# Kernel optimization log

Hardware: AMD Instinct MI355X
Metric: run time of the kernel (lower is better)

Reference implementation:

```python
import jax, jax.numpy as jnp
import numpy as np

N_ATOM_TYPES = 100
N_BOND_TYPES = 10
N_NODES = 10000
N_EDGES = 320000
N_CAND = 100000
HID = 256
N_MP = 3


def setup_inputs() -> dict:
    key = jax.random.key(0)
    ks = jax.random.split(key, 16)
    d = HID
    inp = {
        "atom_types": jax.random.randint(ks[0], (N_NODES,), 0, N_ATOM_TYPES),
        "bond_types": jax.random.randint(ks[1], (N_EDGES,), 0, N_BOND_TYPES),
        "edge_index": jax.random.randint(ks[2], (2, N_EDGES), 0, N_NODES),
        "candidates": jax.random.randint(ks[3], (N_CAND, 2), 0, N_NODES),
        # parameters (weights stored as [in, out]; bias [out])
        "atom_embed": jax.random.normal(ks[4], (N_ATOM_TYPES, d)) * 0.02,
        "atom_W": jax.random.normal(ks[5], (d, d)) / np.sqrt(d),
        "atom_b": jnp.zeros((d,)),
        "bond_embed": jax.random.normal(ks[6], (N_BOND_TYPES, d)) * 0.02,
        "bond_W": jax.random.normal(ks[7], (d, d)) / np.sqrt(d),
        "bond_b": jnp.zeros((d,)),
        "conv_W": jax.random.normal(ks[8], (N_MP, d, d)) / np.sqrt(d),
        "conv_b": jnp.zeros((N_MP, d)),
        "s_W1": jax.random.normal(ks[9], (2 * d, d)) / np.sqrt(2 * d),
        "s_b1": jnp.zeros((d,)),
        "s_W2": jax.random.normal(ks[10], (d, 1)) / np.sqrt(d),
        "s_b2": jnp.zeros((1,)),
    }
    return inp


def _wln_forward(atom_types, bond_types, edge_index, candidates,
                 atom_embed, atom_W, atom_b, bond_embed, bond_W, bond_b,
                 conv_W, conv_b, s_W1, s_b1, s_W2, s_b2):
    # encoders
    h = atom_embed[atom_types] @ atom_W + atom_b            # [N, d]
    e = bond_embed[bond_types] @ bond_W + bond_b            # [E, d] (unused downstream, as in the original forward)
    del e

    src, dst = edge_index[0], edge_index[1]
    n = h.shape[0]
    ones = jnp.ones((src.shape[0],), dtype=h.dtype)
    deg_out = jax.ops.segment_sum(ones, src, num_segments=n)
    deg_in = jax.ops.segment_sum(ones, dst, num_segments=n)
    norm_src = jnp.where(deg_out > 0, deg_out ** -0.5, 0.0)[:, None]  # [N,1]
    norm_dst = jnp.where(deg_in > 0, deg_in ** -0.5, 0.0)[:, None]

    # message passing: DGL GraphConv norm='both' + ReLU
    for i in range(conv_W.shape[0]):
        m = (h * norm_src)[src]                             # [E, d]
        agg = jax.ops.segment_sum(m, dst, num_segments=n)   # [N, d]
        h = jax.nn.relu((agg * norm_dst) @ conv_W[i] + conv_b[i])

    # batched candidate scorer: gather + concat + 2-layer MLP
    u, v = candidates[:, 0], candidates[:, 1]
    pair = jnp.concatenate([h[u], h[v]], axis=-1)           # [C, 2d]
    hid = jax.nn.relu(pair @ s_W1 + s_b1)                   # [C, d]
    scores = hid @ s_W2 + s_b2                              # [C, 1]
    return scores.squeeze(-1)                               # [C]


def reference(atom_types, bond_types, edge_index, candidates,
              atom_embed, atom_W, atom_b, bond_embed, bond_W, bond_b,
              conv_W, conv_b, s_W1, s_b1, s_W2, s_b2):
    return _wln_forward(atom_types, bond_types, edge_index, candidates,
                        atom_embed, atom_W, atom_b, bond_embed, bond_W, bond_b,
                        conv_W, conv_b, s_W1, s_b1, s_W2, s_b2)
```

## Files before the change

kernel.cpp:

```cpp
#include <hip/hip_runtime.h>

#define N_NODES 10000
#define N_EDGES 320000
#define N_CAND  100000
#define HID     256
#define N_MP    3
#define N_ATYPE 100

typedef short bf16x8 __attribute__((ext_vector_type(8)));
typedef float f32x4  __attribute__((ext_vector_type(4)));

static __device__ __forceinline__ float relu_f(float x) { return x > 0.f ? x : 0.f; }

static __device__ __forceinline__ void split_bf16(float s, unsigned short& hi,
                                                  unsigned short& lo)
{
    unsigned u = __float_as_uint(s);
    hi = (unsigned short)(u >> 16);
    float rem = s - __uint_as_float(u & 0xffff0000u);
    unsigned v = __float_as_uint(rem);
    unsigned r = v + 0x7fffu + ((v >> 16) & 1u);
    lo = (unsigned short)(r >> 16);
}

static __device__ __forceinline__ void mfma_tile(
    const unsigned short* __restrict__ Ah, const unsigned short* __restrict__ Al,
    const unsigned short* __restrict__ Wh, const unsigned short* __restrict__ Wl,
    const float* __restrict__ bias, const float* __restrict__ scale,
    float* __restrict__ outF, unsigned short* __restrict__ outH,
    unsigned short* __restrict__ outL,
    int M, int mb, int nb, int doRelu)
{
    int l  = threadIdx.x & 63;
    int li = l & 15;
    int g  = l >> 4;

    int r0 = mb + li;       if (r0 >= M) r0 = M - 1;
    int r1 = mb + 16 + li;  if (r1 >= M) r1 = M - 1;
    int c0 = nb + li;
    int c1 = nb + 16 + li;

    const unsigned short* pA0h = Ah + (size_t)r0 * 256 + g * 8;
    const unsigned short* pA1h = Ah + (size_t)r1 * 256 + g * 8;
    const unsigned short* pA0l = Al + (size_t)r0 * 256 + g * 8;
    const unsigned short* pA1l = Al + (size_t)r1 * 256 + g * 8;
    const unsigned short* pB0h = Wh + (size_t)c0 * 256 + g * 8;
    const unsigned short* pB1h = Wh + (size_t)c1 * 256 + g * 8;
    const unsigned short* pB0l = Wl + (size_t)c0 * 256 + g * 8;
    const unsigned short* pB1l = Wl + (size_t)c1 * 256 + g * 8;

    f32x4 acc00 = {0.f, 0.f, 0.f, 0.f};
    f32x4 acc01 = {0.f, 0.f, 0.f, 0.f};
    f32x4 acc10 = {0.f, 0.f, 0.f, 0.f};
    f32x4 acc11 = {0.f, 0.f, 0.f, 0.f};

    #pragma unroll
    for (int ks = 0; ks < 8; ++ks) {
        int o = ks * 32;
        bf16x8 a0h = *(const bf16x8*)(pA0h + o);
        bf16x8 a1h = *(const bf16x8*)(pA1h + o);
        bf16x8 a0l = *(const bf16x8*)(pA0l + o);
        bf16x8 a1l = *(const bf16x8*)(pA1l + o);
        bf16x8 b0h = *(const bf16x8*)(pB0h + o);
        bf16x8 b1h = *(const bf16x8*)(pB1h + o);
        bf16x8 b0l = *(const bf16x8*)(pB0l + o);
        bf16x8 b1l = *(const bf16x8*)(pB1l + o);

        acc00 = __builtin_amdgcn_mfma_f32_16x16x32_bf16(a0h, b0h, acc00, 0, 0, 0);
        acc01 = __builtin_amdgcn_mfma_f32_16x16x32_bf16(a0h, b1h, acc01, 0, 0, 0);
        acc10 = __builtin_amdgcn_mfma_f32_16x16x32_bf16(a1h, b0h, acc10, 0, 0, 0);
        acc11 = __builtin_amdgcn_mfma_f32_16x16x32_bf16(a1h, b1h, acc11, 0, 0, 0);

        acc00 = __builtin_amdgcn_mfma_f32_16x16x32_bf16(a0h, b0l, acc00, 0, 0, 0);
        acc01 = __builtin_amdgcn_mfma_f32_16x16x32_bf16(a0h, b1l, acc01, 0, 0, 0);
        acc10 = __builtin_amdgcn_mfma_f32_16x16x32_bf16(a1h, b0l, acc10, 0, 0, 0);
        acc11 = __builtin_amdgcn_mfma_f32_16x16x32_bf16(a1h, b1l, acc11, 0, 0, 0);

        acc00 = __builtin_amdgcn_mfma_f32_16x16x32_bf16(a0l, b0h, acc00, 0, 0, 0);
        acc01 = __builtin_amdgcn_mfma_f32_16x16x32_bf16(a0l, b1h, acc01, 0, 0, 0);
        acc10 = __builtin_amdgcn_mfma_f32_16x16x32_bf16(a1l, b0h, acc10, 0, 0, 0);
        acc11 = __builtin_amdgcn_mfma_f32_16x16x32_bf16(a1l, b1h, acc11, 0, 0, 0);
    }

    #pragma unroll
    for (int rt = 0; rt < 2; ++rt) {
        #pragma unroll
        for (int ct = 0; ct < 2; ++ct) {
            f32x4 a = rt ? (ct ? acc11 : acc10) : (ct ? acc01 : acc00);
            int col = nb + ct * 16 + li;
            float bv = bias ? bias[col] : 0.f;
            #pragma unroll
            for (int j = 0; j < 4; ++j) {
                int row = mb + rt * 16 + g * 4 + j;
                if (row >= M) continue;
                float v = a[j] + bv;
                if (doRelu) v = relu_f(v);
                if (scale) v *= scale[row];
                if (outF) {
                    outF[(size_t)row * 256 + col] = v;
                } else {
                    unsigned short hi, lo;
                    split_bf16(v, hi, lo);
                    outH[(size_t)row * 256 + col] = hi;
                    outL[(size_t)row * 256 + col] = lo;
                }
            }
        }
    }
}

static __device__ __forceinline__ void mfma_tile_e0(
    const float* __restrict__ A, const float* __restrict__ B,
    const float* __restrict__ bias, float* __restrict__ C,
    int M, int mb, int nb)
{
    int l  = threadIdx.x & 63;
    int li = l & 15;
    int g  = l >> 4;

    int r0 = mb + li;       if (r0 >= M) r0 = M - 1;
    int r1 = mb + 16 + li;  if (r1 >= M) r1 = M - 1;
    int c0 = nb + li;
    int c1 = nb + 16 + li;

    f32x4 acc00 = {0.f, 0.f, 0.f, 0.f};
    f32x4 acc01 = {0.f, 0.f, 0.f, 0.f};
    f32x4 acc10 = {0.f, 0.f, 0.f, 0.f};
    f32x4 acc11 = {0.f, 0.f, 0.f, 0.f};

    #pragma unroll
    for (int ks = 0; ks < 8; ++ks) {
        int k0 = ks * 32 + g * 8;
        float av0[8], av1[8];
        {
            float4 x0 = *(const float4*)(A + (size_t)r0 * 256 + k0);
            float4 x1 = *(const float4*)(A + (size_t)r0 * 256 + k0 + 4);
            av0[0]=x0.x; av0[1]=x0.y; av0[2]=x0.z; av0[3]=x0.w;
            av0[4]=x1.x; av0[5]=x1.y; av0[6]=x1.z; av0[7]=x1.w;
            float4 y0 = *(const float4*)(A + (size_t)r1 * 256 + k0);
            float4 y1 = *(const float4*)(A + (size_t)r1 * 256 + k0 + 4);
            av1[0]=y0.x; av1[1]=y0.y; av1[2]=y0.z; av1[3]=y0.w;
            av1[4]=y1.x; av1[5]=y1.y; av1[6]=y1.z; av1[7]=y1.w;
        }
        float bv0[8], bv1[8];
        #pragma unroll
        for (int j = 0; j < 8; ++j) {
            bv0[j] = B[(size_t)(k0 + j) * 256 + c0];
            bv1[j] = B[(size_t)(k0 + j) * 256 + c1];
        }
        bf16x8 a0h, a0l, a1h, a1l, b0h, b0l, b1h, b1l;
        #pragma unroll
        for (int j = 0; j < 8; ++j) {
            unsigned short h, lo;
            split_bf16(av0[j], h, lo); a0h[j] = (short)h; a0l[j] = (short)lo;
            split_bf16(av1[j], h, lo); a1h[j] = (short)h; a1l[j] = (short)lo;
            split_bf16(bv0[j], h, lo); b0h[j] = (short)h; b0l[j] = (short)lo;
            split_bf16(bv1[j], h, lo); b1h[j] = (short)h; b1l[j] = (short)lo;
        }

        acc00 = __builtin_amdgcn_mfma_f32_16x16x32_bf16(a0h, b0h, acc00, 0, 0, 0);
        acc01 = __builtin_amdgcn_mfma_f32_16x16x32_bf16(a0h, b1h, acc01, 0, 0, 0);
        acc10 = __builtin_amdgcn_mfma_f32_16x16x32_bf16(a1h, b0h, acc10, 0, 0, 0);
        acc11 = __builtin_amdgcn_mfma_f32_16x16x32_bf16(a1h, b1h, acc11, 0, 0, 0);

        acc00 = __builtin_amdgcn_mfma_f32_16x16x32_bf16(a0h, b0l, acc00, 0, 0, 0);
        acc01 = __builtin_amdgcn_mfma_f32_16x16x32_bf16(a0h, b1l, acc01, 0, 0, 0);
        acc10 = __builtin_amdgcn_mfma_f32_16x16x32_bf16(a1h, b0l, acc10, 0, 0, 0);
        acc11 = __builtin_amdgcn_mfma_f32_16x16x32_bf16(a1h, b1l, acc11, 0, 0, 0);

        acc00 = __builtin_amdgcn_mfma_f32_16x16x32_bf16(a0l, b0h, acc00, 0, 0, 0);
        acc01 = __builtin_amdgcn_mfma_f32_16x16x32_bf16(a0l, b1h, acc01, 0, 0, 0);
        acc10 = __builtin_amdgcn_mfma_f32_16x16x32_bf16(a1l, b0h, acc10, 0, 0, 0);
        acc11 = __builtin_amdgcn_mfma_f32_16x16x32_bf16(a1l, b1h, acc11, 0, 0, 0);
    }

    #pragma unroll
    for (int rt = 0; rt < 2; ++rt) {
        #pragma unroll
        for (int ct = 0; ct < 2; ++ct) {
            f32x4 a = rt ? (ct ? acc11 : acc10) : (ct ? acc01 : acc00);
            int col = nb + ct * 16 + li;
            float bv = bias[col];
            #pragma unroll
            for (int j = 0; j < 4; ++j) {
                int row = mb + rt * 16 + g * 4 + j;
                if (row >= M) continue;
                C[(size_t)row * 256 + col] = a[j] + bv;
            }
        }
    }
}

__global__ __launch_bounds__(256) void k_prep(
    const float* __restrict__ conv_W, const float* __restrict__ s_W1,
    const float* __restrict__ atom_embed, const float* __restrict__ atom_W,
    const float* __restrict__ atom_b,
    unsigned short* __restrict__ WTh, unsigned short* __restrict__ WTl,
    float* __restrict__ E0)
{
    int bid = blockIdx.x;
    if (bid < 80) {
        __shared__ float T[64][65];
        int mat = bid >> 4;
        int t   = bid & 15;
        int ti  = t >> 2;
        int tj  = t & 3;
        const float* src = (mat < 3) ? conv_W + (size_t)mat * 65536
                                     : s_W1 + (size_t)(mat - 3) * 65536;
        #pragma unroll
        for (int i = 0; i < 16; ++i) {
            int flat = i * 256 + threadIdx.x;
            int kr = flat >> 6;
            int nc = flat & 63;
            T[kr][nc] = src[(size_t)(ti * 64 + kr) * 256 + tj * 64 + nc];
        }
        __syncthreads();
        #pragma unroll
        for (int i = 0; i < 16; ++i) {
            int flat = i * 256 + threadIdx.x;
            int nr = flat >> 6;
            int kc = flat & 63;
            unsigned short hi, lo;
            split_bf16(T[kc][nr], hi, lo);
            size_t oi = (size_t)mat * 65536 +
                        (size_t)(tj * 64 + nr) * 256 + ti * 64 + kc;
            WTh[oi] = hi;
            WTl[oi] = lo;
        }
        return;
    }
    int w = (bid - 80) * 4 + (threadIdx.x >> 6);
    if (w < 32) {
        int x = w >> 3, y = w & 7;
        mfma_tile_e0(atom_embed, atom_W, atom_b, E0, N_ATYPE, x * 32, y * 32);
    }
}

__global__ void k_hist(const int* __restrict__ ei,
                       int* __restrict__ dout, int* __restrict__ din)
{
    int e = blockIdx.x * blockDim.x + threadIdx.x;
    if (e >= N_EDGES) return;
    atomicAdd(&dout[ei[e]], 1);
    atomicAdd(&din[ei[N_EDGES + e]], 1);
}

__global__ __launch_bounds__(256) void k_nhs(
    const int* __restrict__ types, const float* __restrict__ E0,
    const int* __restrict__ dout, const int* __restrict__ din,
    float* __restrict__ ns, float* __restrict__ nd, float* __restrict__ h,
    int* __restrict__ off)
{
    if (blockIdx.x == 2500) {
        __shared__ int part[256];
        int t = threadIdx.x;
        const int chunk = 40;
        int base = t * chunk;
        int s = 0;
        for (int i = 0; i < chunk; ++i) {
            int idx = base + i;
            if (idx < N_NODES) s += din[idx];
        }
        part[t] = s;
        __syncthreads();
        for (int d = 1; d < 256; d <<= 1) {
            int v = (t >= d) ? part[t - d] : 0;
            __syncthreads();
            part[t] += v;
            __syncthreads();
        }
        int run = (t == 0) ? 0 : part[t - 1];
        if (t == 0) off[0] = 0;
        for (int i = 0; i < chunk; ++i) {
            int idx = base + i;
            if (idx < N_NODES) { run += din[idx]; off[idx + 1] = run; }
        }
        return;
    }
    int node = blockIdx.x * 4 + (threadIdx.x >> 6);
    int lane = threadIdx.x & 63;
    if (node >= N_NODES) return;
    int o  = dout[node];
    int in = din[node];
    float nsv = (o  > 0) ? (1.0f / sqrtf((float)o))  : 0.f;
    float ndv = (in > 0) ? (1.0f / sqrtf((float)in)) : 0.f;
    if (lane == 0) { ns[node] = nsv; nd[node] = ndv; }
    int t = types[node];
    float4 v = ((const float4*)E0)[(size_t)t * 64 + lane];
    v.x *= nsv; v.y *= nsv; v.z *= nsv; v.w *= nsv;
    ((float4*)h)[(size_t)node * 64 + lane] = v;
}

__global__ void k_fill(const int* __restrict__ ei, const int* __restrict__ off,
                       int* __restrict__ cur, int* __restrict__ csr)
{
    int e = blockIdx.x * blockDim.x + threadIdx.x;
    if (e >= N_EDGES) return;
    int d = ei[N_EDGES + e];
    int p = off[d] + atomicAdd(&cur[d], 1);
    csr[p] = ei[e];
}

__global__ __launch_bounds__(256) void k_agg(
    const float* __restrict__ h, const float* __restrict__ nd,
    const int* __restrict__ off, const int* __restrict__ csr,
    unsigned short* __restrict__ Ah, unsigned short* __restrict__ Al)
{
    int bid  = blockIdx.x;
    int slot = bid & 7;
    int c    = slot >> 1;
    int p    = ((bid >> 3) << 1) | (slot & 1);
    int wave = threadIdx.x >> 6;
    int lane = threadIdx.x & 63;
    int wi   = p * 4 + wave;
    int col  = c * 64 + lane;

    for (int node = wi; node < N_NODES; node += 2048) {
        int s0 = off[node], s1 = off[node + 1];
        float a0 = 0.f, a1 = 0.f, a2 = 0.f, a3 = 0.f;
        float a4 = 0.f, a5 = 0.f, a6 = 0.f, a7 = 0.f;
        int e = s0;
        for (; e + 8 <= s1; e += 8) {
            int i0 = csr[e],     i1 = csr[e + 1], i2 = csr[e + 2], i3 = csr[e + 3];
            int i4 = csr[e + 4], i5 = csr[e + 5], i6 = csr[e + 6], i7 = csr[e + 7];
            float v0 = h[(size_t)i0 * 256 + col];
            float v1 = h[(size_t)i1 * 256 + col];
            float v2 = h[(size_t)i2 * 256 + col];
            float v3 = h[(size_t)i3 * 256 + col];
            float v4 = h[(size_t)i4 * 256 + col];
            float v5 = h[(size_t)i5 * 256 + col];
            float v6 = h[(size_t)i6 * 256 + col];
            float v7 = h[(size_t)i7 * 256 + col];
            a0 += v0; a1 += v1; a2 += v2; a3 += v3;
            a4 += v4; a5 += v5; a6 += v6; a7 += v7;
        }
        for (; e < s1; ++e)
            a0 += h[(size_t)csr[e] * 256 + col];
        float s = (((a0 + a1) + (a2 + a3)) + ((a4 + a5) + (a6 + a7))) * nd[node];
        unsigned short hi, lo;
        split_bf16(s, hi, lo);
        Ah[(size_t)node * 256 + col] = hi;
        Al[(size_t)node * 256 + col] = lo;
    }
}

__global__ __launch_bounds__(256) void k_conv(
    const unsigned short* __restrict__ Ah, const unsigned short* __restrict__ Al,
    const unsigned short* __restrict__ Wh, const unsigned short* __restrict__ Wl,
    const float* __restrict__ bias, const float* __restrict__ scale,
    float* __restrict__ outF, unsigned short* __restrict__ outH,
    unsigned short* __restrict__ outL, int M, int isLast)
{
    int t = blockIdx.x * 4 + (threadIdx.x >> 6);
    int x = t >> 3, y = t & 7;
    if (x * 32 >= M) return;
    if (isLast)
        mfma_tile(Ah, Al, Wh, Wl, bias, nullptr, nullptr, outH, outL,
                  M, x * 32, y * 32, 1);
    else
        mfma_tile(Ah, Al, Wh, Wl, bias, scale, outF, nullptr, nullptr,
                  M, x * 32, y * 32, 1);
}

__global__ __launch_bounds__(256) void k_pq(
    const unsigned short* __restrict__ Ah, const unsigned short* __restrict__ Al,
    const unsigned short* __restrict__ WTh, const unsigned short* __restrict__ WTl,
    float* __restrict__ P, float* __restrict__ Q, int M)
{
    int t = blockIdx.x * 4 + (threadIdx.x >> 6);
    if (t >= 313 * 16) return;
    int x = t >> 4, r = t & 15;
    int half = r >> 3, y = r & 7;
    if (x * 32 >= M) return;
    const unsigned short* wh = WTh + (size_t)(3 + half) * 65536;
    const unsigned short* wl = WTl + (size_t)(3 + half) * 65536;
    mfma_tile(Ah, Al, wh, wl, nullptr, nullptr,
              half ? Q : P, nullptr, nullptr, M, x * 32, y * 32, 0);
}

__global__ __launch_bounds__(256) void k_score_part(
    const int* __restrict__ cand, const float* __restrict__ P,
    const float* __restrict__ Q, const float* __restrict__ b1,
    const float* __restrict__ W2, float* __restrict__ part)
{
    int bid = blockIdx.x;
    int c   = bid & 7;
    int grp = bid >> 3;
    int cd  = grp * 256 + threadIdx.x;
    if (cd >= N_CAND) return;

    int u = cand[2 * cd];
    int v = cand[2 * cd + 1];
    const float4* P4 = (const float4*)P;
    const float4* Q4 = (const float4*)Q;
    const float4* B4 = (const float4*)b1;
    const float4* W4 = (const float4*)W2;
    size_t pb = (size_t)u * 64 + c * 8;
    size_t qb = (size_t)v * 64 + c * 8;

    float4 p[8], q[8];
    #pragma unroll
    for (int i = 0; i < 8; ++i) p[i] = P4[pb + i];
    #pragma unroll
    for (int i = 0; i < 8; ++i) q[i] = Q4[qb + i];

    float acc = 0.f;
    #pragma unroll
    for (int i = 0; i < 8; ++i) {
        float4 b = B4[c * 8 + i];
        float4 w = W4[c * 8 + i];
        acc = fmaf(relu_f(p[i].x + q[i].x + b.x), w.x, acc);
        acc = fmaf(relu_f(p[i].y + q[i].y + b.y), w.y, acc);
        acc = fmaf(relu_f(p[i].z + q[i].z + b.z), w.z, acc);
        acc = fmaf(relu_f(p[i].w + q[i].w + b.w), w.w, acc);
    }
    part[(size_t)c * N_CAND + cd] = acc;
}

__global__ void k_sred(const float* __restrict__ part,
                       const float* __restrict__ b2, float* __restrict__ out)
{
    int i = blockIdx.x * 256 + threadIdx.x;
    if (i >= N_CAND) return;
    float s = b2[0];
    #pragma unroll
    for (int c = 0; c < 8; ++c) s += part[(size_t)c * N_CAND + i];
    out[i] = s;
}

extern "C" void kernel_launch(void* const* d_in, const int* in_sizes, int n_in,
                              void* d_out, int out_size, void* d_ws, size_t ws_size,
                              hipStream_t stream)
{
    const int*   atom_types = (const int*)d_in[0];
    const int*   edge_index = (const int*)d_in[2];
    const int*   candidates = (const int*)d_in[3];
    const float* atom_embed = (const float*)d_in[4];
    const float* atom_W     = (const float*)d_in[5];
    const float* atom_b     = (const float*)d_in[6];
    const float* conv_W     = (const float*)d_in[10];
    const float* conv_b     = (const float*)d_in[11];
    const float* s_W1       = (const float*)d_in[12];
    const float* s_b1       = (const float*)d_in[13];
    const float* s_W2       = (const float*)d_in[14];
    const float* s_b2       = (const float*)d_in[15];
    float* out = (float*)d_out;

    char* w = (char*)d_ws;
    size_t o = 0;
    auto alloc = [&](size_t bytes) {
        void* p = w + o;
        o += (bytes + 255) & ~(size_t)255;
        return p;
    };
    int*            ints = (int*)alloc((size_t)3 * N_NODES * 4);
    float*          h0   = (float*)alloc((size_t)N_NODES * HID * 4);
    float*          h1   = (float*)alloc((size_t)N_NODES * HID * 4);
    float*          Pm   = (float*)alloc((size_t)N_NODES * HID * 4);
    float*          Qm   = (float*)alloc((size_t)N_NODES * HID * 4);
    unsigned short* Ah   = (unsigned short*)alloc((size_t)N_NODES * HID * 2);
    unsigned short* Al   = (unsigned short*)alloc((size_t)N_NODES * HID * 2);
    unsigned short* Ah2  = (unsigned short*)alloc((size_t)N_NODES * HID * 2);
    unsigned short* Al2  = (unsigned short*)alloc((size_t)N_NODES * HID * 2);
    unsigned short* WTh  = (unsigned short*)alloc((size_t)5 * 65536 * 2);
    unsigned short* WTl  = (unsigned short*)alloc((size_t)5 * 65536 * 2);
    float*          E0   = (float*)alloc((size_t)N_ATYPE * HID * 4);
    float*          part = (float*)alloc((size_t)8 * N_CAND * 4);
    float*          ns   = (float*)alloc((size_t)N_NODES * 4);
    float*          nd   = (float*)alloc((size_t)N_NODES * 4);
    int*            off  = (int*)alloc((size_t)(N_NODES + 1) * 4);
    int*            csr  = (int*)alloc((size_t)N_EDGES * 4);
    int* dego = ints;
    int* degi = ints + N_NODES;
    int* cur  = ints + 2 * N_NODES;

    hipMemsetAsync(ints, 0, (size_t)3 * N_NODES * 4, stream);

    k_hist<<<1250, 256, 0, stream>>>(edge_index, dego, degi);
    k_prep<<<88, 256, 0, stream>>>(conv_W, s_W1, atom_embed, atom_W, atom_b,
                                   WTh, WTl, E0);
    k_nhs<<<2501, 256, 0, stream>>>(atom_types, E0, dego, degi, ns, nd, h0, off);
    k_fill<<<(N_EDGES + 255) / 256, 256, 0, stream>>>(edge_index, off, cur, csr);

    const float* hc = h0;
    float* hn = h1;
    for (int L = 0; L < N_MP; ++L) {
        k_agg<<<2048, 256, 0, stream>>>(hc, nd, off, csr, Ah, Al);
        int isLast = (L == N_MP - 1);
        k_conv<<<628, 256, 0, stream>>>(
            Ah, Al, WTh + (size_t)L * 65536, WTl + (size_t)L * 65536,
            conv_b + (size_t)L * HID, ns, hn, Ah2, Al2, N_NODES, isLast);
        float* t = (float*)hc; hc = hn; hn = t;
    }
    k_pq<<<1252, 256, 0, stream>>>(Ah2, Al2, WTh, WTl, Pm, Qm, N_NODES);

    k_score_part<<<3128, 256, 0, stream>>>(candidates, Pm, Qm, s_b1, s_W2, part);
    k_sred<<<(N_CAND + 255) / 256, 256, 0, stream>>>(part, s_b2, out);
}
```

Baseline: 345.9 us.

## Fuse last conv layer with P/Q projection via LDS and merge histogram into prep

The final GraphConv layer and the scorer's P/Q projections now run in one kernel. Each 512-thread block computes a 32-row ReLU'd conv tile, splits it into hi/lo bf16 in shared memory with a swizzled layout, then multiplies it by both halves of s_W1. This removes the global round trip of the intermediate Ah2/Al2 buffers and one launch. The degree histogram also moves into the prep kernel's grid to save another launch. In exchange, the fused kernel launches only 313 blocks, which may leave CUs underused, and it uses 32KB of LDS per block.

```diff
diff --git a/kernel.cpp b/kernel.cpp
--- a/kernel.cpp
+++ b/kernel.cpp
@@ -23,13 +23,16 @@
     lo = (unsigned short)(r >> 16);
 }
 
+static __device__ __forceinline__ int swz_blk(int rloc, int blk)
+{
+    return blk ^ (rloc & 7) ^ ((rloc & 3) << 3);
+}
+
 static __device__ __forceinline__ void mfma_tile(
     const unsigned short* __restrict__ Ah, const unsigned short* __restrict__ Al,
     const unsigned short* __restrict__ Wh, const unsigned short* __restrict__ Wl,
     const float* __restrict__ bias, const float* __restrict__ scale,
-    float* __restrict__ outF, unsigned short* __restrict__ outH,
-    unsigned short* __restrict__ outL,
-    int M, int mb, int nb, int doRelu)
+    float* __restrict__ outF, int M, int mb, int nb, int doRelu)
 {
     int l  = threadIdx.x & 63;
     int li = l & 15;
@@ -96,14 +99,7 @@
                 float v = a[j] + bv;
                 if (doRelu) v = relu_f(v);
                 if (scale) v *= scale[row];
-                if (outF) {
-                    outF[(size_t)row * 256 + col] = v;
-                } else {
-                    unsigned short hi, lo;
-                    split_bf16(v, hi, lo);
-                    outH[(size_t)row * 256 + col] = hi;
-                    outL[(size_t)row * 256 + col] = lo;
-                }
+                outF[(size_t)row * 256 + col] = v;
             }
         }
     }
@@ -194,9 +190,9 @@
 __global__ __launch_bounds__(256) void k_prep(
     const float* __restrict__ conv_W, const float* __restrict__ s_W1,
     const float* __restrict__ atom_embed, const float* __restrict__ atom_W,
-    const float* __restrict__ atom_b,
+    const float* __restrict__ atom_b, const int* __restrict__ ei,
     unsigned short* __restrict__ WTh, unsigned short* __restrict__ WTl,
-    float* __restrict__ E0)
+    float* __restrict__ E0, int* __restrict__ dout, int* __restrict__ din)
 {
     int bid = blockIdx.x;
     if (bid < 80) {
@@ -227,22 +223,18 @@
             WTh[oi] = hi;
             WTl[oi] = lo;
         }
-        return;
-    }
-    int w = (bid - 80) * 4 + (threadIdx.x >> 6);
-    if (w < 32) {
-        int x = w >> 3, y = w & 7;
-        mfma_tile_e0(atom_embed, atom_W, atom_b, E0, N_ATYPE, x * 32, y * 32);
-    }
-}
-
-__global__ void k_hist(const int* __restrict__ ei,
-                       int* __restrict__ dout, int* __restrict__ din)
-{
-    int e = blockIdx.x * blockDim.x + threadIdx.x;
-    if (e >= N_EDGES) return;
-    atomicAdd(&dout[ei[e]], 1);
-    atomicAdd(&din[ei[N_EDGES + e]], 1);
+    } else if (bid < 88) {
+        int w = (bid - 80) * 4 + (threadIdx.x >> 6);
+        if (w < 32) {
+            int x = w >> 3, y = w & 7;
+            mfma_tile_e0(atom_embed, atom_W, atom_b, E0, N_ATYPE, x * 32, y * 32);
+        }
+    }
+    int gidx = bid * 256 + threadIdx.x;
+    if (gidx < N_EDGES) {
+        atomicAdd(&dout[ei[gidx]], 1);
+        atomicAdd(&din[ei[N_EDGES + gidx]], 1);
+    }
 }
 
 __global__ __launch_bounds__(256) void k_nhs(
@@ -348,34 +340,173 @@
     const unsigned short* __restrict__ Ah, const unsigned short* __restrict__ Al,
     const unsigned short* __restrict__ Wh, const unsigned short* __restrict__ Wl,
     const float* __restrict__ bias, const float* __restrict__ scale,
-    float* __restrict__ outF, unsigned short* __restrict__ outH,
-    unsigned short* __restrict__ outL, int M, int isLast)
+    float* __restrict__ outF, int M)
 {
     int t = blockIdx.x * 4 + (threadIdx.x >> 6);
     int x = t >> 3, y = t & 7;
     if (x * 32 >= M) return;
-    if (isLast)
-        mfma_tile(Ah, Al, Wh, Wl, bias, nullptr, nullptr, outH, outL,
-                  M, x * 32, y * 32, 1);
-    else
-        mfma_tile(Ah, Al, Wh, Wl, bias, scale, outF, nullptr, nullptr,
-                  M, x * 32, y * 32, 1);
-}
-
-__global__ __launch_bounds__(256) void k_pq(
+    mfma_tile(Ah, Al, Wh, Wl, bias, scale, outF, M, x * 32, y * 32, 1);
+}
+
+__global__ __launch_bounds__(512) void k_convpq(
     const unsigned short* __restrict__ Ah, const unsigned short* __restrict__ Al,
+    const unsigned short* __restrict__ Wch, const unsigned short* __restrict__ Wcl,
+    const float* __restrict__ bias,
     const unsigned short* __restrict__ WTh, const unsigned short* __restrict__ WTl,
     float* __restrict__ P, float* __restrict__ Q, int M)
 {
-    int t = blockIdx.x * 4 + (threadIdx.x >> 6);
-    if (t >= 313 * 16) return;
-    int x = t >> 4, r = t & 15;
-    int half = r >> 3, y = r & 7;
-    if (x * 32 >= M) return;
-    const unsigned short* wh = WTh + (size_t)(3 + half) * 65536;
-    const unsigned short* wl = WTl + (size_t)(3 + half) * 65536;
-    mfma_tile(Ah, Al, wh, wl, nullptr, nullptr,
-              half ? Q : P, nullptr, nullptr, M, x * 32, y * 32, 0);
+    __shared__ unsigned short Lh[32 * 256];
+    __shared__ unsigned short Ll[32 * 256];
+
+    int w  = threadIdx.x >> 6;
+    int l  = threadIdx.x & 63;
+    int li = l & 15;
+    int g  = l >> 4;
+    int mb = blockIdx.x * 32;
+
+    if (mb + 32 > M) {
+        for (int f = threadIdx.x; f < 32 * 256; f += 512) {
+            int r = f >> 8;
+            if (mb + r >= M) { Lh[f] = 0; Ll[f] = 0; }
+        }
+    }
+
+    {
+        int nb = w * 32;
+        int r0 = mb + li;       if (r0 >= M) r0 = M - 1;
+        int r1 = mb + 16 + li;  if (r1 >= M) r1 = M - 1;
+        int c0 = nb + li;
+        int c1 = nb + 16 + li;
+
+        const unsigned short* pA0h = Ah + (size_t)r0 * 256 + g * 8;
+        const unsigned short* pA1h = Ah + (size_t)r1 * 256 + g * 8;
+        const unsigned short* pA0l = Al + (size_t)r0 * 256 + g * 8;
+        const unsigned short* pA1l = Al + (size_t)r1 * 256 + g * 8;
+        const unsigned short* pB0h = Wch + (size_t)c0 * 256 + g * 8;
+        const unsigned short* pB1h = Wch + (size_t)c1 * 256 + g * 8;
+        const unsigned short* pB0l = Wcl + (size_t)c0 * 256 + g * 8;
+        const unsigned short* pB1l = Wcl + (size_t)c1 * 256 + g * 8;
+
+        f32x4 acc00 = {0.f, 0.f, 0.f, 0.f};
+        f32x4 acc01 = {0.f, 0.f, 0.f, 0.f};
+        f32x4 acc10 = {0.f, 0.f, 0.f, 0.f};
+        f32x4 acc11 = {0.f, 0.f, 0.f, 0.f};
+
+        #pragma unroll
+        for (int ks = 0; ks < 8; ++ks) {
+            int o = ks * 32;
+            bf16x8 a0h = *(const bf16x8*)(pA0h + o);
+            bf16x8 a1h = *(const bf16x8*)(pA1h + o);
+            bf16x8 a0l = *(const bf16x8*)(pA0l + o);
+            bf16x8 a1l = *(const bf16x8*)(pA1l + o);
+            bf16x8 b0h = *(const bf16x8*)(pB0h + o);
+            bf16x8 b1h = *(const bf16x8*)(pB1h + o);
+            bf16x8 b0l = *(const bf16x8*)(pB0l + o);
+            bf16x8 b1l = *(const bf16x8*)(pB1l + o);
+
+            acc00 = __builtin_amdgcn_mfma_f32_16x16x32_bf16(a0h, b0h, acc00, 0, 0, 0);
+            acc01 = __builtin_amdgcn_mfma_f32_16x16x32_bf16(a0h, b1h, acc01, 0, 0, 0);
+            acc10 = __builtin_amdgcn_mfma_f32_16x16x32_bf16(a1h, b0h, acc10, 0, 0, 0);
+            acc11 = __builtin_amdgcn_mfma_f32_16x16x32_bf16(a1h, b1h, acc11, 0, 0, 0);
+
+            acc00 = __builtin_amdgcn_mfma_f32_16x16x32_bf16(a0h, b0l, acc00, 0, 0, 0);
+            acc01 = __builtin_amdgcn_mfma_f32_16x16x32_bf16(a0h, b1l, acc01, 0, 0, 0);
+            acc10 = __builtin_amdgcn_mfma_f32_16x16x32_bf16(a1h, b0l, acc10, 0, 0, 0);
+            acc11 = __builtin_amdgcn_mfma_f32_16x16x32_bf16(a1h, b1l, acc11, 0, 0, 0);
+
+            acc00 = __builtin_amdgcn_mfma_f32_16x16x32_bf16(a0l, b0h, acc00, 0, 0, 0);
+            acc01 = __builtin_amdgcn_mfma_f32_16x16x32_bf16(a0l, b1h, acc01, 0, 0, 0);
+            acc10 = __builtin_amdgcn_mfma_f32_16x16x32_bf16(a1l, b0h, acc10, 0, 0, 0);
+            acc11 = __builtin_amdgcn_mfma_f32_16x16x32_bf16(a1l, b1h, acc11, 0, 0, 0);
+        }
+
+        #pragma unroll
+        for (int rt = 0; rt < 2; ++rt) {
+            #pragma unroll
+            for (int ct = 0; ct < 2; ++ct) {
+                f32x4 a = rt ? (ct ? acc11 : acc10) : (ct ? acc01 : acc00);
+                int col = nb + ct * 16 + li;
+                float bv = bias[col];
+                #pragma unroll
+                for (int j = 0; j < 4; ++j) {
+                    int rloc = rt * 16 + g * 4 + j;
+                    if (mb + rloc >= M) continue;
+                    float v = relu_f(a[j] + bv);
+                    unsigned short hi, lo;
+                    split_bf16(v, hi, lo);
+                    int blk2 = swz_blk(rloc, col >> 3);
+                    int addr = rloc * 256 + blk2 * 8 + (col & 7);
+                    Lh[addr] = hi;
+                    Ll[addr] = lo;
+                }
+            }
+        }
+    }
+    __syncthreads();
+
+    #pragma unroll
+    for (int it = 0; it < 2; ++it) {
+        int t = w + it * 8;
+        int half = t >> 3;
+        int y    = t & 7;
+        const unsigned short* Bh = WTh + (size_t)(3 + half) * 65536;
+        const unsigned short* Bl = WTl + (size_t)(3 + half) * 65536;
+        float* C = half ? Q : P;
+        int nb = y * 32;
+        int c0 = nb + li;
+        int c1 = nb + 16 + li;
+
+        f32x4 acc00 = {0.f, 0.f, 0.f, 0.f};
+        f32x4 acc01 = {0.f, 0.f, 0.f, 0.f};
+        f32x4 acc10 = {0.f, 0.f, 0.f, 0.f};
+        f32x4 acc11 = {0.f, 0.f, 0.f, 0.f};
+
+        #pragma unroll
+        for (int ks = 0; ks < 8; ++ks) {
+            int blk = ks * 4 + g;
+            int b0 = swz_blk(li, blk);
+            bf16x8 a0h = *(const bf16x8*)(&Lh[li * 256 + b0 * 8]);
+            bf16x8 a0l = *(const bf16x8*)(&Ll[li * 256 + b0 * 8]);
+            bf16x8 a1h = *(const bf16x8*)(&Lh[(16 + li) * 256 + b0 * 8]);
+            bf16x8 a1l = *(const bf16x8*)(&Ll[(16 + li) * 256 + b0 * 8]);
+
+            int o = ks * 32 + g * 8;
+            bf16x8 b0h = *(const bf16x8*)(Bh + (size_t)c0 * 256 + o);
+            bf16x8 b1h = *(const bf16x8*)(Bh + (size_t)c1 * 256 + o);
+            bf16x8 b0l = *(const bf16x8*)(Bl + (size_t)c0 * 256 + o);
+            bf16x8 b1l = *(const bf16x8*)(Bl + (size_t)c1 * 256 + o);
+
+            acc00 = __builtin_amdgcn_mfma_f32_16x16x32_bf16(a0h, b0h, acc00, 0, 0, 0);
+            acc01 = __builtin_amdgcn_mfma_f32_16x16x32_bf16(a0h, b1h, acc01, 0, 0, 0);
+            acc10 = __builtin_amdgcn_mfma_f32_16x16x32_bf16(a1h, b0h, acc10, 0, 0, 0);
+            acc11 = __builtin_amdgcn_mfma_f32_16x16x32_bf16(a1h, b1h, acc11, 0, 0, 0);
+
+            acc00 = __builtin_amdgcn_mfma_f32_16x16x32_bf16(a0h, b0l, acc00, 0, 0, 0);
+            acc01 = __builtin_amdgcn_mfma_f32_16x16x32_bf16(a0h, b1l, acc01, 0, 0, 0);
+            acc10 = __builtin_amdgcn_mfma_f32_16x16x32_bf16(a1h, b0l, acc10, 0, 0, 0);
+            acc11 = __builtin_amdgcn_mfma_f32_16x16x32_bf16(a1h, b1l, acc11, 0, 0, 0);
+
+            acc00 = __builtin_amdgcn_mfma_f32_16x16x32_bf16(a0l, b0h, acc00, 0, 0, 0);
+            acc01 = __builtin_amdgcn_mfma_f32_16x16x32_bf16(a0l, b1h, acc01, 0, 0, 0);
+            acc10 = __builtin_amdgcn_mfma_f32_16x16x32_bf16(a1l, b0h, acc10, 0, 0, 0);
+            acc11 = __builtin_amdgcn_mfma_f32_16x16x32_bf16(a1l, b1h, acc11, 0, 0, 0);
+        }
+
+        #pragma unroll
+        for (int rt = 0; rt < 2; ++rt) {
+            #pragma unroll
+            for (int ct = 0; ct < 2; ++ct) {
+                f32x4 a = rt ? (ct ? acc11 : acc10) : (ct ? acc01 : acc00);
+                int col = nb + ct * 16 + li;
+                #pragma unroll
+                for (int j = 0; j < 4; ++j) {
+                    int row = mb + rt * 16 + g * 4 + j;
+                    if (row >= M) continue;
+                    C[(size_t)row * 256 + col] = a[j];
+                }
+            }
+        }
+    }
 }
 
 __global__ __launch_bounds__(256) void k_score_part(
@@ -460,8 +591,6 @@
     float*          Qm   = (float*)alloc((size_t)N_NODES * HID * 4);
     unsigned short* Ah   = (unsigned short*)alloc((size_t)N_NODES * HID * 2);
     unsigned short* Al   = (unsigned short*)alloc((size_t)N_NODES * HID * 2);
-    unsigned short* Ah2  = (unsigned short*)alloc((size_t)N_NODES * HID * 2);
-    unsigned short* Al2  = (unsigned short*)alloc((size_t)N_NODES * HID * 2);
     unsigned short* WTh  = (unsigned short*)alloc((size_t)5 * 65536 * 2);
     unsigned short* WTl  = (unsigned short*)alloc((size_t)5 * 65536 * 2);
     float*          E0   = (float*)alloc((size_t)N_ATYPE * HID * 4);
@@ -476,23 +605,24 @@
 
     hipMemsetAsync(ints, 0, (size_t)3 * N_NODES * 4, stream);
 
-    k_hist<<<1250, 256, 0, stream>>>(edge_index, dego, degi);
-    k_prep<<<88, 256, 0, stream>>>(conv_W, s_W1, atom_embed, atom_W, atom_b,
-                                   WTh, WTl, E0);
+    k_prep<<<1280, 256, 0, stream>>>(conv_W, s_W1, atom_embed, atom_W, atom_b,
+                                     edge_index, WTh, WTl, E0, dego, degi);
     k_nhs<<<2501, 256, 0, stream>>>(atom_types, E0, dego, degi, ns, nd, h0, off);
     k_fill<<<(N_EDGES + 255) / 256, 256, 0, stream>>>(edge_index, off, cur, csr);
 
     const float* hc = h0;
     float* hn = h1;
-    for (int L = 0; L < N_MP; ++L) {
+    for (int L = 0; L < 2; ++L) {
         k_agg<<<2048, 256, 0, stream>>>(hc, nd, off, csr, Ah, Al);
-        int isLast = (L == N_MP - 1);
         k_conv<<<628, 256, 0, stream>>>(
             Ah, Al, WTh + (size_t)L * 65536, WTl + (size_t)L * 65536,
-            conv_b + (size_t)L * HID, ns, hn, Ah2, Al2, N_NODES, isLast);
+            conv_b + (size_t)L * HID, ns, hn, N_NODES);
         float* t = (float*)hc; hc = hn; hn = t;
     }
-    k_pq<<<1252, 256, 0, stream>>>(Ah2, Al2, WTh, WTl, Pm, Qm, N_NODES);
+    k_agg<<<2048, 256, 0, stream>>>(hc, nd, off, csr, Ah, Al);
+    k_convpq<<<313, 512, 0, stream>>>(
+        Ah, Al, WTh + (size_t)2 * 65536, WTl + (size_t)2 * 65536,
+        conv_b + (size_t)2 * HID, WTh, WTl, Pm, Qm, N_NODES);
 
     k_score_part<<<3128, 256, 0, stream>>>(candidates, Pm, Qm, s_b1, s_W2, part);
     k_sred<<<(N_CAND + 255) / 256, 256, 0, stream>>>(part, s_b2, out);
```

Result: faster. 335.1 us, median of 2 (-3.1%).
